# Kernel tuning notes

Measured on AMD Instinct MI355X. Metric: run time of the kernel, lower is better.

Reference implementation:

```python
import jax, jax.numpy as jnp
import numpy as np

E, C, K, S = 8, 128, 512, 512  # embedding_dim, channels, kernel_size, stride
NEG_SLOPE = 0.01  # torch F.leaky_relu default


def setup_inputs() -> dict:
    key = jax.random.key(0)
    ks = jax.random.split(key, 11)
    B, T = 4, 1_000_000
    sc = 0.05
    return {
        "x": jax.random.normal(ks[0], (B, T, E), jnp.float32),
        # ctx_conv: Conv1d(E, 2C, K, stride=S) -> weight (2C, E, K), bias (2C,)
        "ctx_conv_w": jax.random.normal(ks[1], (2 * C, E, K), jnp.float32) * sc,
        "ctx_conv_b": jax.random.normal(ks[2], (2 * C,), jnp.float32) * sc,
        # ctx_share: Conv1d(C, C, 1) -> (C, C) pointwise
        "ctx_share_w": jax.random.normal(ks[3], (C, C), jnp.float32) * sc,
        "ctx_share_b": jax.random.normal(ks[4], (C,), jnp.float32) * sc,
        "main_conv_w": jax.random.normal(ks[5], (2 * C, E, K), jnp.float32) * sc,
        "main_conv_b": jax.random.normal(ks[6], (2 * C,), jnp.float32) * sc,
        "main_share_w": jax.random.normal(ks[7], (C, C), jnp.float32) * sc,
        "main_share_b": jax.random.normal(ks[8], (C,), jnp.float32) * sc,
        # gct_proj: Linear(C, C) -> weight (C, C) (y = g @ W.T + b)
        "gct_proj_w": jax.random.normal(ks[9], (C, C), jnp.float32) * sc,
        "gct_proj_b": jax.random.normal(ks[10], (C,), jnp.float32) * sc,
    }


def _leaky(x):
    return jnp.where(x >= 0, x, NEG_SLOPE * x)


def _glu(x):  # GLU over channel dim 1
    a, b = jnp.split(x, 2, axis=1)
    return a * jax.nn.sigmoid(b)


def _conv(z, w, b):
    # z: (B, Cin, T), w: (Cout, Cin, K) -> (B, Cout, T_out), stride S, VALID
    y = jax.lax.conv_general_dilated(z, w, (S,), 'VALID',
                                     dimension_numbers=('NCH', 'OIH', 'NCH'))
    return y + b[None, :, None]


def _branch_act(z, wc, bc, ws, bs):
    # glu(conv(z)) -> leaky_relu(1x1 share conv)
    h = _glu(_conv(z, wc, bc))                                   # (B, C, T_out)
    h = _leaky(jnp.einsum('oc,bct->bot', ws, h) + bs[None, :, None])
    return h


def reference(x, ctx_conv_w, ctx_conv_b, ctx_share_w, ctx_share_b,
              main_conv_w, main_conv_b, main_share_w, main_share_b,
              gct_proj_w, gct_proj_b):
    z = jnp.transpose(x, (0, 2, 1))  # (B, E, T)
    # Context branch: global max over time of ctx activations (GCG context).
    g = _branch_act(z, ctx_conv_w, ctx_conv_b, ctx_share_w, ctx_share_b)
    gct = jnp.max(g, axis=-1)  # (B, C)
    # Main branch with global channel gating.
    h = _branch_act(z, main_conv_w, main_conv_b, main_share_w, main_share_b)  # (B, C, T_out)
    q = jnp.tanh(gct @ gct_proj_w.T + gct_proj_b)                # (B, C)
    gate = jax.nn.sigmoid(jnp.einsum('bct,bc->bt', h, q))        # (B, T_out)
    out = jnp.max(h * gate[:, None, :], axis=-1)                 # (B, C)
    return out
```

## Files before the change

### kernel.cpp

```cpp
#include <hip/hip_runtime.h>
#include <hip/hip_bf16.h>
#include <cmath>

#define B_    4
#define T_    1000000
#define E_    8
#define C_    128
#define NCH   512
#define KK    4096
#define TOUT  1953
#define TP    1956
#define TPAD  2048
#define NT2   31

typedef __attribute__((ext_vector_type(8))) short bf16x8;
typedef __attribute__((ext_vector_type(4))) float f32x4;

__device__ __forceinline__ float sigmoidf_(float v) { return 1.f / (1.f + __expf(-v)); }

__global__ __launch_bounds__(256) void prep_inputs(
    const float* __restrict__ x,
    const float* __restrict__ wc, const float* __restrict__ bc,
    const float* __restrict__ wm, const float* __restrict__ bm,
    __hip_bfloat16* __restrict__ xb2, __hip_bfloat16* __restrict__ Wn2,
    float* __restrict__ bias_t) {
  __shared__ float row[KK];
  const int bid = blockIdx.x;
  if (bid < NCH) {
    const int n = bid, br = n >> 8, o = n & 255;
    const float* wsrc = (br ? wm : wc) + (size_t)o * KK;
    for (int i = threadIdx.x; i < KK; i += 256) row[i] = wsrc[i];
    __syncthreads();
    const int nt = n >> 4, nr = n & 15;
    for (int k = threadIdx.x; k < KK; k += 256) {
      int kpos = k >> 3, e = k & 7;
      size_t addr = (((size_t)nt * 128 + (k >> 5)) * 64
                     + (size_t)((k >> 3) & 3) * 16 + nr) * 8 + (k & 7);
      Wn2[addr] = __float2bfloat16(row[e * 512 + kpos]);
    }
    if (threadIdx.x == 0) bias_t[n] = (br ? bm : bc)[o];
  } else {
    size_t gid = (size_t)(bid - NCH) * 256 + threadIdx.x;
    size_t idx8 = gid * 8;
    size_t b = idx8 >> 23, rem = idx8 & ((1ull << 23) - 1);
    int lane = (int)((rem >> 3) & 63);
    int kc   = (int)((rem >> 9) & 127);
    int tt   = (int)(rem >> 16);
    int t = tt * 16 + (lane & 15);
    int k = kc * 32 + (lane >> 4) * 8;
    union { __hip_bfloat16 h[8]; uint4 u; } o;
    if (t < TOUT) {
      const float* src = x + b * 8000000ull + (size_t)t * KK + k;
      float4 f0 = *(const float4*)(src);
      float4 f1 = *(const float4*)(src + 4);
      o.h[0] = __float2bfloat16(f0.x); o.h[1] = __float2bfloat16(f0.y);
      o.h[2] = __float2bfloat16(f0.z); o.h[3] = __float2bfloat16(f0.w);
      o.h[4] = __float2bfloat16(f1.x); o.h[5] = __float2bfloat16(f1.y);
      o.h[6] = __float2bfloat16(f1.z); o.h[7] = __float2bfloat16(f1.w);
    } else {
      o.u = make_uint4(0, 0, 0, 0);
    }
    *(uint4*)(xb2 + idx8) = o.u;
  }
}

__global__ __launch_bounds__(512, 2) void mfma_gemm(
    const __hip_bfloat16* __restrict__ xb2, const __hip_bfloat16* __restrict__ Wn2,
    float* __restrict__ u2) {
  const int tid  = threadIdx.x;
  const int lane = tid & 63, wave = tid >> 6;
  const int wt = wave & 3, wn = wave >> 2;

  const int L   = blockIdx.x;
  const int xcd = L & 7;
  const int r   = L >> 3;
  const int nb  = r & 3;
  const int sh  = r >> 2;
  const int s   = sh * 8 + xcd;
  const int tblk = s & 15, b = s >> 4;
  const int t0 = tblk * 128, n0 = nb * 128;

  const size_t FR = 512;
  const __hip_bfloat16* aB = xb2
      + ((size_t)(b * 128 + (t0 >> 4) + wt * 2) * 128) * FR + (size_t)lane * 8;
  const __hip_bfloat16* bB = Wn2
      + ((size_t)((n0 >> 4) + wn * 4) * 128) * FR + (size_t)lane * 8;

  f32x4 acc[2][4];
#pragma unroll
  for (int i = 0; i < 2; ++i)
#pragma unroll
    for (int j = 0; j < 4; ++j) acc[i][j] = (f32x4)(0.0f);

  bf16x8 A0[2][2], B0[4][2], A1[2][2], B1[4][2];

  auto load_set = [&](bf16x8 (&aF)[2][2], bf16x8 (&bF)[4][2], int kc) {
#pragma unroll
    for (int i = 0; i < 2; ++i)
#pragma unroll
      for (int c = 0; c < 2; ++c)
        aF[i][c] = *(const bf16x8*)(aB + (size_t)(i * 128 + kc + c) * FR);
#pragma unroll
    for (int j = 0; j < 4; ++j)
#pragma unroll
      for (int c = 0; c < 2; ++c)
        bF[j][c] = *(const bf16x8*)(bB + (size_t)(j * 128 + kc + c) * FR);
  };
  auto do_mfma = [&](bf16x8 (&aF)[2][2], bf16x8 (&bF)[4][2]) {
#pragma unroll
    for (int c = 0; c < 2; ++c)
#pragma unroll
      for (int i = 0; i < 2; ++i)
#pragma unroll
        for (int j = 0; j < 4; ++j)
          acc[i][j] = __builtin_amdgcn_mfma_f32_16x16x32_bf16(aF[i][c], bF[j][c],
                                                              acc[i][j], 0, 0, 0);
  };

  load_set(A0, B0, 0);
  for (int kc = 0; kc < 128; kc += 4) {
    load_set(A1, B1, kc + 2);
    do_mfma(A0, B0);
    if (kc + 4 < 128) load_set(A0, B0, kc + 4);
    do_mfma(A1, B1);
  }

  const int crow = (lane >> 4) * 4;
  const int ccol = lane & 15;
#pragma unroll
  for (int j = 0; j < 4; ++j) {
    int n = n0 + wn * 64 + j * 16 + ccol;
    float* urow = u2 + ((size_t)n * B_ + b) * TP;
#pragma unroll
    for (int i = 0; i < 2; ++i) {
      int t = t0 + wt * 32 + i * 16 + crow;
      if (t < TOUT) *(f32x4*)(urow + t) = acc[i][j];
    }
  }
}

__global__ __launch_bounds__(256) void share_act(
    const float* __restrict__ u2, const float* __restrict__ bias_t,
    const float* __restrict__ wsc, const float* __restrict__ bsc,
    const float* __restrict__ wsm, const float* __restrict__ bsm,
    float* __restrict__ hmain, float* __restrict__ gct_part) {
  __shared__ float Wl[128 * 132];
  __shared__ float ul[128 * 68];
  const int tid  = threadIdx.x;
  const int tile = blockIdx.x;
  const int b    = blockIdx.y;
  const int br   = blockIdx.z;
  const int t0   = tile * 64;
  const float* ws = br ? wsm : wsc;
  const float* bs = br ? bsm : bsc;

  for (int g = tid; g < 16384; g += 256) {
    int co = g >> 7, cp = g & 127;
    Wl[cp * 132 + co] = ws[g];
  }
  const size_t base_v = ((size_t)(br * 256) * B_ + b) * TP;
  const size_t base_g = ((size_t)(br * 256 + 128) * B_ + b) * TP;
  for (int g = tid; g < 8192; g += 256) {
    int cp = g >> 6, t = g & 63;
    float v = 0.f;
    if (t0 + t < TOUT) {
      float va = u2[base_v + (size_t)cp * B_ * TP + t0 + t] + bias_t[br * 256 + cp];
      float vg = u2[base_g + (size_t)cp * B_ * TP + t0 + t] + bias_t[br * 256 + 128 + cp];
      v = va * sigmoidf_(vg);
    }
    ul[cp * 68 + t] = v;
  }
  __syncthreads();

  const int ty = tid >> 4, tx = tid & 15;
  float acc[8][4];
#pragma unroll
  for (int i = 0; i < 8; ++i)
#pragma unroll
    for (int j = 0; j < 4; ++j) acc[i][j] = 0.f;

  for (int cp = 0; cp < 128; ++cp) {
    float4 a0 = *(const float4*)&Wl[cp*132 + ty*4];
    float4 a1 = *(const float4*)&Wl[cp*132 + 64 + ty*4];
    float4 b4 = *(const float4*)&ul[cp*68 + tx*4];
    float av[8] = {a0.x,a0.y,a0.z,a0.w,a1.x,a1.y,a1.z,a1.w};
    float bv[4] = {b4.x,b4.y,b4.z,b4.w};
#pragma unroll
    for (int i = 0; i < 8; ++i)
#pragma unroll
      for (int j = 0; j < 4; ++j) acc[i][j] = fmaf(av[i], bv[j], acc[i][j]);
  }

  float mloc[8];
#pragma unroll
  for (int i = 0; i < 8; ++i) mloc[i] = -INFINITY;
#pragma unroll
  for (int i = 0; i < 8; ++i) {
    int c = (i < 4) ? (ty*4 + i) : (64 + ty*4 + (i - 4));
    float bias = bs[c];
#pragma unroll
    for (int j = 0; j < 4; ++j) {
      int t = t0 + tx*4 + j;
      if (t >= TOUT) continue;
      float v = acc[i][j] + bias;
      v = (v >= 0.f) ? v : 0.01f * v;
      if (br == 1) {
        hmain[((size_t)b * 128 + c) * TOUT + t] = v;
      } else {
        mloc[i] = fmaxf(mloc[i], v);
      }
    }
  }
  if (br == 0) {
    __syncthreads();
    float* red = ul;
#pragma unroll
    for (int i = 0; i < 8; ++i) {
      int c = (i < 4) ? (ty*4 + i) : (64 + ty*4 + (i - 4));
      red[c * 16 + tx] = mloc[i];
    }
    __syncthreads();
    if (tid < 128) {
      float m = -INFINITY;
#pragma unroll
      for (int k = 0; k < 16; ++k) m = fmaxf(m, red[tid * 16 + k]);
      gct_part[((size_t)b * 128 + tid) * NT2 + tile] = m;
    }
  }
}

__global__ void gct_q(const float* __restrict__ gct_part, const float* __restrict__ wp,
                      const float* __restrict__ bp, float* __restrict__ q) {
  int b = blockIdx.x, tid = threadIdx.x;
  __shared__ float g[128];
  float m = -INFINITY;
  for (int tl = 0; tl < NT2; ++tl) m = fmaxf(m, gct_part[((size_t)b * 128 + tid) * NT2 + tl]);
  g[tid] = m;
  __syncthreads();
  float s = bp[tid];
  for (int c = 0; c < 128; ++c) s = fmaf(g[c], wp[tid * 128 + c], s);
  q[b * 128 + tid] = tanhf(s);
}

__global__ __launch_bounds__(256) void gate_max(
    const float* __restrict__ hmain, const float* __restrict__ q,
    float* __restrict__ out_part) {
  __shared__ float hl[128 * 68];
  __shared__ float ql[128];
  __shared__ float red[256];
  __shared__ float gl[64];
  int tid = threadIdx.x, tile = blockIdx.x, b = blockIdx.y;
  int t0 = tile * 64;
  for (int g = tid; g < 8192; g += 256) {
    int c = g >> 6, t = g & 63;
    hl[c * 68 + t] = (t0 + t < TOUT) ? hmain[((size_t)b * 128 + c) * TOUT + t0 + t] : 0.f;
  }
  if (tid < 128) ql[tid] = q[b * 128 + tid];
  __syncthreads();
  {
    int t = tid & 63, cy = tid >> 6;
    float s = 0.f;
#pragma unroll
    for (int cc = 0; cc < 32; ++cc) s = fmaf(hl[(cy * 32 + cc) * 68 + t], ql[cy * 32 + cc], s);
    red[cy * 64 + t] = s;
  }
  __syncthreads();
  if (tid < 64) {
    float s = red[tid] + red[64 + tid] + red[128 + tid] + red[192 + tid];
    gl[tid] = sigmoidf_(s);
  }
  __syncthreads();
  {
    int c = tid >> 1, th = tid & 1;
    float m = -INFINITY;
#pragma unroll
    for (int tt = 0; tt < 32; ++tt) {
      int t = th * 32 + tt;
      if (t0 + t < TOUT) m = fmaxf(m, hl[c * 68 + t] * gl[t]);
    }
    red[c * 2 + th] = m;
  }
  __syncthreads();
  if (tid < 128) out_part[((size_t)b * 128 + tid) * NT2 + tile] = fmaxf(red[tid * 2], red[tid * 2 + 1]);
}

__global__ void final_max(const float* __restrict__ out_part, float* __restrict__ out) {
  int idx = blockIdx.x * 256 + threadIdx.x;
  if (idx < 512) {
    float m = -INFINITY;
    for (int tl = 0; tl < NT2; ++tl) m = fmaxf(m, out_part[(size_t)idx * NT2 + tl]);
    out[idx] = m;
  }
}

extern "C" void kernel_launch(void* const* d_in, const int* in_sizes, int n_in,
                              void* d_out, int out_size, void* d_ws, size_t ws_size,
                              hipStream_t stream) {
  const float* x      = (const float*)d_in[0];
  const float* ctx_w  = (const float*)d_in[1];
  const float* ctx_b  = (const float*)d_in[2];
  const float* ctx_sw = (const float*)d_in[3];
  const float* ctx_sb = (const float*)d_in[4];
  const float* main_w = (const float*)d_in[5];
  const float* main_b = (const float*)d_in[6];
  const float* main_sw= (const float*)d_in[7];
  const float* main_sb= (const float*)d_in[8];
  const float* gp_w   = (const float*)d_in[9];
  const float* gp_b   = (const float*)d_in[10];

  char* w = (char*)d_ws;
  __hip_bfloat16* xb2 = (__hip_bfloat16*)(w);
  __hip_bfloat16* Wn2 = (__hip_bfloat16*)(w + 67108864);
  float* bias_t  = (float*)(w + 71303168);
  float* u2      = (float*)(w + 71305216);
  float* hmain   = (float*)(w + 87328768);
  float* gct_part= (float*)(w + 91328512);
  float* q       = (float*)(w + 91392000);
  float* out_part= (float*)(w + 91394048);

  prep_inputs<<<NCH + 16384, 256, 0, stream>>>(x, ctx_w, ctx_b, main_w, main_b,
                                               xb2, Wn2, bias_t);
  mfma_gemm<<<256, 512, 0, stream>>>(xb2, Wn2, u2);
  share_act<<<dim3(NT2, B_, 2), 256, 0, stream>>>(u2, bias_t, ctx_sw, ctx_sb,
                                                  main_sw, main_sb, hmain, gct_part);
  gct_q<<<B_, 128, 0, stream>>>(gct_part, gp_w, gp_b, q);
  gate_max<<<dim3(NT2, B_), 256, 0, stream>>>(hmain, q, out_part);
  final_max<<<2, 256, 0, stream>>>(out_part, (float*)d_out);
}
```

Before: 314.6 us.

## Stage GEMM operand tiles into LDS via async global_load_lds double buffering

The MFMA GEMM previously had every wave load its A and B fragments straight from global memory, so tiles shared across waves were fetched redundantly. Each wave now issues direct global-to-LDS loads for a quarter of the shared tile into a double-buffered LDS array, and all waves read their fragments from LDS. This cuts global/L2 traffic at the cost of 64 KB of LDS per block and a barrier per k-step, which may limit occupancy and serialize the pipeline.

Result: no change. 309.4 us (-1.6%).

```diff
diff --git a/kernel.cpp b/kernel.cpp
--- a/kernel.cpp
+++ b/kernel.cpp
@@ -17,6 +17,12 @@
 typedef __attribute__((ext_vector_type(4))) float f32x4;
 
 __device__ __forceinline__ float sigmoidf_(float v) { return 1.f / (1.f + __expf(-v)); }
+
+__device__ __forceinline__ void gload_lds16(const __hip_bfloat16* g, __hip_bfloat16* l) {
+  __builtin_amdgcn_global_load_lds(
+      (const __attribute__((address_space(1))) void*)(const void*)g,
+      (__attribute__((address_space(3))) void*)(void*)l, 16, 0, 0);
+}
 
 __global__ __launch_bounds__(256) void prep_inputs(
     const float* __restrict__ x,
@@ -67,6 +73,8 @@
 __global__ __launch_bounds__(512, 2) void mfma_gemm(
     const __hip_bfloat16* __restrict__ xb2, const __hip_bfloat16* __restrict__ Wn2,
     float* __restrict__ u2) {
+  __shared__ __hip_bfloat16 lds[2][16384];
+
   const int tid  = threadIdx.x;
   const int lane = tid & 63, wave = tid >> 6;
   const int wt = wave & 3, wn = wave >> 2;
@@ -81,10 +89,21 @@
   const int t0 = tblk * 128, n0 = nb * 128;
 
   const size_t FR = 512;
-  const __hip_bfloat16* aB = xb2
-      + ((size_t)(b * 128 + (t0 >> 4) + wt * 2) * 128) * FR + (size_t)lane * 8;
-  const __hip_bfloat16* bB = Wn2
-      + ((size_t)((n0 >> 4) + wn * 4) * 128) * FR + (size_t)lane * 8;
+
+  const __hip_bfloat16* gsrc[4];
+  int cslot[4];
+#pragma unroll
+  for (int s2 = 0; s2 < 4; ++s2) {
+    int c = wave * 4 + s2;
+    cslot[c & 3] = c;
+    if (c < 16) {
+      gsrc[s2] = xb2 + ((size_t)(b * 128 + tblk * 8 + (c >> 1)) * 128 + (c & 1)) * FR
+                 + (size_t)lane * 8;
+    } else {
+      gsrc[s2] = Wn2 + ((size_t)(nb * 8 + ((c - 16) >> 1)) * 128 + (c & 1)) * FR
+                 + (size_t)lane * 8;
+    }
+  }
 
   f32x4 acc[2][4];
 #pragma unroll
@@ -92,21 +111,27 @@
 #pragma unroll
     for (int j = 0; j < 4; ++j) acc[i][j] = (f32x4)(0.0f);
 
-  bf16x8 A0[2][2], B0[4][2], A1[2][2], B1[4][2];
-
-  auto load_set = [&](bf16x8 (&aF)[2][2], bf16x8 (&bF)[4][2], int kc) {
+  auto STAGE = [&](int buf, int step) {
+#pragma unroll
+    for (int s2 = 0; s2 < 4; ++s2) {
+      gload_lds16(gsrc[s2] + (size_t)step * 1024, &lds[buf][(size_t)cslot[s2] * FR]);
+    }
+  };
+
+  auto COMPUTE = [&](int buf) {
+    bf16x8 aF[2][2], bF[4][2];
 #pragma unroll
     for (int i = 0; i < 2; ++i)
 #pragma unroll
       for (int c = 0; c < 2; ++c)
-        aF[i][c] = *(const bf16x8*)(aB + (size_t)(i * 128 + kc + c) * FR);
+        aF[i][c] = *(const bf16x8*)(&lds[buf][(size_t)((wt * 2 + i) * 2 + c) * FR
+                                              + (size_t)lane * 8]);
 #pragma unroll
     for (int j = 0; j < 4; ++j)
 #pragma unroll
       for (int c = 0; c < 2; ++c)
-        bF[j][c] = *(const bf16x8*)(bB + (size_t)(j * 128 + kc + c) * FR);
-  };
-  auto do_mfma = [&](bf16x8 (&aF)[2][2], bf16x8 (&bF)[4][2]) {
+        bF[j][c] = *(const bf16x8*)(&lds[buf][(size_t)(16 + (wn * 4 + j) * 2 + c) * FR
+                                              + (size_t)lane * 8]);
 #pragma unroll
     for (int c = 0; c < 2; ++c)
 #pragma unroll
@@ -117,12 +142,16 @@
                                                               acc[i][j], 0, 0, 0);
   };
 
-  load_set(A0, B0, 0);
-  for (int kc = 0; kc < 128; kc += 4) {
-    load_set(A1, B1, kc + 2);
-    do_mfma(A0, B0);
-    if (kc + 4 < 128) load_set(A0, B0, kc + 4);
-    do_mfma(A1, B1);
+  STAGE(0, 0);
+  __syncthreads();
+
+  int cur = 0;
+#pragma unroll 1
+  for (int step = 0; step < 64; ++step) {
+    if (step + 1 < 64) STAGE(cur ^ 1, step + 1);
+    COMPUTE(cur);
+    __syncthreads();
+    cur ^= 1;
   }
 
   const int crow = (lane >> 4) * 4;
```
